# Optimization experiments

Hardware: AMD Instinct MI355X
Metric: run time of the kernel (lower is better)

The kernel has to match this reference:

```python
import jax, jax.numpy as jnp
import numpy as np

N = 8192
D = 128
NUM_CLASSES = 16
EPS = 1e-8  # torch cosine_similarity eps


def setup_inputs() -> dict:
    key = jax.random.key(0)
    k1, k2 = jax.random.split(key)
    inp = jax.random.normal(k1, (N, D), dtype=jnp.float32)
    targets = jax.random.randint(k2, (N,), 0, NUM_CLASSES, dtype=jnp.int64)
    temperature = jnp.asarray(0.5, dtype=jnp.float32)
    return {"input": inp, "targets": targets, "temperature": temperature}


def reference(input, targets, temperature):
    # clamp temperature to [0.1, 1.0] as the module does in forward
    temp = jnp.clip(temperature, 0.1, 1.0)

    # cosine similarity matrix [N, N]
    norms = jnp.maximum(jnp.linalg.norm(input, axis=1, keepdims=True), EPS)
    xn = input / norms
    sim = jnp.matmul(xn, xn.T) / temp          # [N, N]
    E = jnp.exp(sim)                            # [N, N]

    same = targets[:, None] == targets[None, :]  # [N, N] bool
    diag = jnp.diagonal(E)                       # exp(s_ii)
    pos = jnp.sum(jnp.where(same, E, 0.0), axis=1) - diag   # same-class, excl self
    tot = jnp.sum(E, axis=1) - diag                          # pos + neg
    per_sample_loss = -jnp.log(pos / tot)                    # [N]

    # per-class aggregation (segment sums with static num_segments)
    counts = jax.ops.segment_sum(jnp.ones_like(per_sample_loss), targets,
                                 num_segments=NUM_CLASSES)
    sums = jax.ops.segment_sum(per_sample_loss, targets,
                               num_segments=NUM_CLASSES)
    safe_counts = jnp.maximum(counts, 1.0)
    class_mean = sums / safe_counts

    # class weights: (1/count) normalized over present classes
    inv = jnp.where(counts > 0, 1.0 / safe_counts, 0.0)
    weights = inv / jnp.sum(inv)

    # only classes with more than one sample contribute
    valid = counts > 1
    weighted = jnp.where(valid, class_mean * weights, 0.0)
    n_valid = jnp.sum(valid.astype(jnp.float32))
    loss = jnp.sum(weighted) / n_valid
    return loss
```

## Files before the change

### kernel.cpp

```cpp
#include <hip/hip_runtime.h>

#define N 8192
#define D 128
#define NCLS 16
#define SLOT 512
#define RSTRIDE 256

typedef unsigned short u16;
typedef __attribute__((ext_vector_type(8))) short v8s;
typedef __attribute__((ext_vector_type(16))) float f32x16;

static __device__ inline u16 f2bf(float f) {
  unsigned int u = __builtin_bit_cast(unsigned int, f);
  unsigned int r = u + 0x7fffu + ((u >> 16) & 1u);
  return (u16)(r >> 16);
}

__global__ __launch_bounds__(256) void k_norm(float* __restrict__ buf) {
  int wave = threadIdx.x >> 6;
  int lane = threadIdx.x & 63;
  int row = blockIdx.x * 4 + wave;
  const float* p = buf + (size_t)row * D + lane * 2;
  float x = p[0], y = p[1];
  float ss = x * x + y * y;
#pragma unroll
  for (int m = 32; m >= 1; m >>= 1) ss += __shfl_xor(ss, m);
  float nrm = fmaxf(sqrtf(ss), 1e-8f);
  float inv = 1.0f / nrm;
  unsigned int u0 = (unsigned int)f2bf(x * inv);
  unsigned int u1 = (unsigned int)f2bf(y * inv);
  reinterpret_cast<unsigned int*>(buf)[(size_t)row * 128 + lane] = u0 | (u1 << 16);
}

__global__ __launch_bounds__(256, 2) void k_sim(float* __restrict__ buf,
                                                const int* __restrict__ tgt,
                                                const float* __restrict__ temp) {
  const int tid = threadIdx.x;
  const int wave = tid >> 6;
  const int lane = tid & 63;
  const int l31 = lane & 31;
  const int h = lane >> 5;

  const u16* xnb = reinterpret_cast<const u16*>(buf);

  const int bid = blockIdx.x;
  const int rowstrip = bid >> 2;
  const int cq = bid & 3;
  const int rwb = rowstrip * 64 + (wave >> 1) * 32;
  const int cbase = cq * 2048 + (wave & 1) * 32;

  float t = temp[0];
  t = fminf(fmaxf(t, 0.1f), 1.0f);
  const float scale = 1.4426950408889634f / t;

  v8s afrag[8];
  {
    const u16* ap = xnb + (size_t)(rwb + l31) * RSTRIDE + h * 8;
#pragma unroll
    for (int kk = 0; kk < 8; ++kk)
      afrag[kk] = *reinterpret_cast<const v8s*>(ap + kk * 16);
  }

  int trow[16];
#pragma unroll
  for (int r = 0; r < 16; ++r)
    trow[r] = tgt[rwb + ((r & 3) + 8 * (r >> 2) + 4 * h)];

  float tot_acc[16], pos_acc[16];
#pragma unroll
  for (int r = 0; r < 16; ++r) { tot_acc[r] = 0.f; pos_acc[r] = 0.f; }

  const u16* bp = xnb + (size_t)(cbase + l31) * RSTRIDE + h * 8;

  v8s bA[8], bB[8];
#pragma unroll
  for (int kk = 0; kk < 8; ++kk) bA[kk] = *reinterpret_cast<const v8s*>(bp + kk * 16);
#pragma unroll
  for (int kk = 0; kk < 8; ++kk) bB[kk] = *reinterpret_cast<const v8s*>(bp + 64 * RSTRIDE + kk * 16);

  auto tileCompute = [&](const v8s (&bf)[8], int c0) {
    f32x16 acc;
#pragma unroll
    for (int r = 0; r < 16; ++r) acc[r] = 0.f;
#pragma unroll
    for (int kk = 0; kk < 8; ++kk)
      acc = __builtin_amdgcn_mfma_f32_32x32x16_bf16(afrag[kk], bf[kk], acc, 0, 0, 0);
    int tcol = tgt[c0 + l31];
    if (c0 != rwb) {
#pragma unroll
      for (int r = 0; r < 16; ++r) {
        float e = exp2f(acc[r] * scale);
        tot_acc[r] += e;
        pos_acc[r] += (tcol == trow[r]) ? e : 0.f;
      }
    } else {
#pragma unroll
      for (int r = 0; r < 16; ++r) {
        float e = exp2f(acc[r] * scale);
        if (l31 == ((r & 3) + 8 * (r >> 2) + 4 * h)) e = 0.f;
        tot_acc[r] += e;
        pos_acc[r] += (tcol == trow[r]) ? e : 0.f;
      }
    }
  };

  for (int tt = 0; tt < 32; tt += 2) {
    tileCompute(bA, cbase + tt * 64);
    if (tt + 2 < 32) {
      const u16* q = bp + (size_t)(tt + 2) * 64 * RSTRIDE;
#pragma unroll
      for (int kk = 0; kk < 8; ++kk) bA[kk] = *reinterpret_cast<const v8s*>(q + kk * 16);
    }
    tileCompute(bB, cbase + (tt + 1) * 64);
    if (tt + 3 < 32) {
      const u16* q = bp + (size_t)(tt + 3) * 64 * RSTRIDE;
#pragma unroll
      for (int kk = 0; kk < 8; ++kk) bB[kk] = *reinterpret_cast<const v8s*>(q + kk * 16);
    }
  }

  __shared__ float red_pos[4][32];
  __shared__ float red_tot[4][32];
#pragma unroll
  for (int r = 0; r < 16; ++r) {
    float p = pos_acc[r], q = tot_acc[r];
#pragma unroll
    for (int m = 1; m <= 16; m <<= 1) {
      p += __shfl_xor(p, m);
      q += __shfl_xor(q, m);
    }
    if (l31 == 0) {
      int rl = (r & 3) + 8 * (r >> 2) + 4 * h;
      red_pos[wave][rl] = p;
      red_tot[wave][rl] = q;
    }
  }
  __syncthreads();
  if (tid < 64) {
    int g = tid >> 5, rl = tid & 31;
    int row = rowstrip * 64 + g * 32 + rl;
    float p = red_pos[2 * g][rl] + red_pos[2 * g + 1][rl];
    float q = red_tot[2 * g][rl] + red_tot[2 * g + 1][rl];
    float* slot = reinterpret_cast<float*>(reinterpret_cast<char*>(buf) + (size_t)row * SLOT + 256);
    slot[cq] = p;
    slot[4 + cq] = q;
  }
}

__global__ __launch_bounds__(128) void k_rowloss(float* __restrict__ buf,
                                                 const int* __restrict__ tgt) {
  __shared__ float cs[NCLS], cc[NCLS];
  int tid = threadIdx.x;
  int i = blockIdx.x * 128 + tid;
  if (tid < NCLS) { cs[tid] = 0.f; cc[tid] = 0.f; }
  __syncthreads();
  const float* slot = reinterpret_cast<const float*>(reinterpret_cast<const char*>(buf) + (size_t)i * SLOT + 256);
  float pos = slot[0] + slot[1] + slot[2] + slot[3];
  float tot = slot[4] + slot[5] + slot[6] + slot[7];
  float loss = logf(tot) - logf(pos);
  int c = tgt[i];
  atomicAdd(&cs[c], loss);
  atomicAdd(&cc[c], 1.0f);
  __syncthreads();
  if (tid < NCLS) {
    float* cls = reinterpret_cast<float*>(reinterpret_cast<char*>(buf) + (size_t)blockIdx.x * SLOT);
    cls[80 + tid] = cs[tid];
    cls[96 + tid] = cc[tid];
  }
}

__global__ __launch_bounds__(64) void k_final(const float* __restrict__ buf,
                                              float* __restrict__ out) {
  int c = threadIdx.x;
  float s = 0.f, n = 0.f;
  if (c < NCLS) {
#pragma unroll 4
    for (int b = 0; b < N / 128; ++b) {
      const float* cls = reinterpret_cast<const float*>(reinterpret_cast<const char*>(buf) + (size_t)b * SLOT);
      s += cls[80 + c];
      n += cls[96 + c];
    }
  }
  float safe = fmaxf(n, 1.0f);
  float mean = s / safe;
  float inv = (n > 0.5f) ? 1.0f / safe : 0.f;
  float valid = (n > 1.5f) ? 1.f : 0.f;
  float w = valid * mean * inv;
  float sinv = inv, sw = w, sv = valid;
#pragma unroll
  for (int m = 1; m <= 32; m <<= 1) {
    sinv += __shfl_xor(sinv, m);
    sw += __shfl_xor(sw, m);
    sv += __shfl_xor(sv, m);
  }
  if (c == 0) out[0] = sw / sinv / sv;
}

extern "C" void kernel_launch(void* const* d_in, const int* in_sizes, int n_in,
                              void* d_out, int out_size, void* d_ws, size_t ws_size,
                              hipStream_t stream) {
  float* buf = (float*)d_in[0];
  const int* tgt = (const int*)d_in[1];
  const float* temp = (const float*)d_in[2];
  float* out = (float*)d_out;
  (void)d_ws; (void)ws_size;

  k_norm<<<N / 4, 256, 0, stream>>>(buf);
  k_sim<<<512, 256, 0, stream>>>(buf, tgt, temp);
  k_rowloss<<<N / 128, 128, 0, stream>>>(buf, tgt);
  k_final<<<1, 64, 0, stream>>>(buf, out);
}
```

Baseline: 138.4 us.

## Fold temperature into normalization, retile sim kernel, fuse loss tail kernels

The normalization kernel now multiplies each row by sqrt(log2(e)/temp), so the sim kernel feeds the MFMA accumulators straight into exp2 with no per-element multiply. The sim kernel moves to 512-thread blocks covering 128 rows by 1024 columns, giving 8 column partials per row. The row-loss and final-reduction kernels merge into a single 1024-thread kernel, removing one launch and its round trip through global memory. The launch bound of (512, 4) caps registers hard, which can cause spills given the large fragment arrays. The folded scale is also rounded to bf16 along with the data, which slightly changes precision.

```diff
diff --git a/kernel.cpp b/kernel.cpp
--- a/kernel.cpp
+++ b/kernel.cpp
@@ -16,7 +16,8 @@
   return (u16)(r >> 16);
 }
 
-__global__ __launch_bounds__(256) void k_norm(float* __restrict__ buf) {
+__global__ __launch_bounds__(256) void k_norm(float* __restrict__ buf,
+                                              const float* __restrict__ temp) {
   int wave = threadIdx.x >> 6;
   int lane = threadIdx.x & 63;
   int row = blockIdx.x * 4 + wave;
@@ -25,16 +26,16 @@
   float ss = x * x + y * y;
 #pragma unroll
   for (int m = 32; m >= 1; m >>= 1) ss += __shfl_xor(ss, m);
-  float nrm = fmaxf(sqrtf(ss), 1e-8f);
-  float inv = 1.0f / nrm;
+  float t = fminf(fmaxf(temp[0], 0.1f), 1.0f);
+  float sc = sqrtf(1.4426950408889634f / t);
+  float inv = sc / fmaxf(sqrtf(ss), 1e-8f);
   unsigned int u0 = (unsigned int)f2bf(x * inv);
   unsigned int u1 = (unsigned int)f2bf(y * inv);
   reinterpret_cast<unsigned int*>(buf)[(size_t)row * 128 + lane] = u0 | (u1 << 16);
 }
 
-__global__ __launch_bounds__(256, 2) void k_sim(float* __restrict__ buf,
-                                                const int* __restrict__ tgt,
-                                                const float* __restrict__ temp) {
+__global__ __launch_bounds__(512, 4) void k_sim(float* __restrict__ buf,
+                                                const int* __restrict__ tgt) {
   const int tid = threadIdx.x;
   const int wave = tid >> 6;
   const int lane = tid & 63;
@@ -44,14 +45,10 @@
   const u16* xnb = reinterpret_cast<const u16*>(buf);
 
   const int bid = blockIdx.x;
-  const int rowstrip = bid >> 2;
-  const int cq = bid & 3;
-  const int rwb = rowstrip * 64 + (wave >> 1) * 32;
-  const int cbase = cq * 2048 + (wave & 1) * 32;
-
-  float t = temp[0];
-  t = fminf(fmaxf(t, 0.1f), 1.0f);
-  const float scale = 1.4426950408889634f / t;
+  const int rowstrip = bid >> 3;
+  const int cq = bid & 7;
+  const int rwb = rowstrip * 128 + (wave >> 1) * 32;
+  const int cbase = cq * 1024 + (wave & 1) * 32;
 
   v8s afrag[8];
   {
@@ -76,7 +73,7 @@
 #pragma unroll
   for (int kk = 0; kk < 8; ++kk) bA[kk] = *reinterpret_cast<const v8s*>(bp + kk * 16);
 #pragma unroll
-  for (int kk = 0; kk < 8; ++kk) bB[kk] = *reinterpret_cast<const v8s*>(bp + 64 * RSTRIDE + kk * 16);
+  for (int kk = 0; kk < 8; ++kk) bB[kk] = *reinterpret_cast<const v8s*>(bp + (size_t)64 * RSTRIDE + kk * 16);
 
   auto tileCompute = [&](const v8s (&bf)[8], int c0) {
     f32x16 acc;
@@ -89,14 +86,14 @@
     if (c0 != rwb) {
 #pragma unroll
       for (int r = 0; r < 16; ++r) {
-        float e = exp2f(acc[r] * scale);
+        float e = exp2f(acc[r]);
         tot_acc[r] += e;
         pos_acc[r] += (tcol == trow[r]) ? e : 0.f;
       }
     } else {
 #pragma unroll
       for (int r = 0; r < 16; ++r) {
-        float e = exp2f(acc[r] * scale);
+        float e = exp2f(acc[r]);
         if (l31 == ((r & 3) + 8 * (r >> 2) + 4 * h)) e = 0.f;
         tot_acc[r] += e;
         pos_acc[r] += (tcol == trow[r]) ? e : 0.f;
@@ -104,23 +101,23 @@
     }
   };
 
-  for (int tt = 0; tt < 32; tt += 2) {
+  for (int tt = 0; tt < 16; tt += 2) {
     tileCompute(bA, cbase + tt * 64);
-    if (tt + 2 < 32) {
+    if (tt + 2 < 16) {
       const u16* q = bp + (size_t)(tt + 2) * 64 * RSTRIDE;
 #pragma unroll
       for (int kk = 0; kk < 8; ++kk) bA[kk] = *reinterpret_cast<const v8s*>(q + kk * 16);
     }
     tileCompute(bB, cbase + (tt + 1) * 64);
-    if (tt + 3 < 32) {
+    if (tt + 3 < 16) {
       const u16* q = bp + (size_t)(tt + 3) * 64 * RSTRIDE;
 #pragma unroll
       for (int kk = 0; kk < 8; ++kk) bB[kk] = *reinterpret_cast<const v8s*>(q + kk * 16);
     }
   }
 
-  __shared__ float red_pos[4][32];
-  __shared__ float red_tot[4][32];
+  __shared__ float red_pos[8][32];
+  __shared__ float red_tot[8][32];
 #pragma unroll
   for (int r = 0; r < 16; ++r) {
     float p = pos_acc[r], q = tot_acc[r];
@@ -136,64 +133,56 @@
     }
   }
   __syncthreads();
-  if (tid < 64) {
+  if (tid < 128) {
     int g = tid >> 5, rl = tid & 31;
-    int row = rowstrip * 64 + g * 32 + rl;
+    int row = rowstrip * 128 + g * 32 + rl;
     float p = red_pos[2 * g][rl] + red_pos[2 * g + 1][rl];
     float q = red_tot[2 * g][rl] + red_tot[2 * g + 1][rl];
     float* slot = reinterpret_cast<float*>(reinterpret_cast<char*>(buf) + (size_t)row * SLOT + 256);
     slot[cq] = p;
-    slot[4 + cq] = q;
-  }
-}
-
-__global__ __launch_bounds__(128) void k_rowloss(float* __restrict__ buf,
-                                                 const int* __restrict__ tgt) {
+    slot[8 + cq] = q;
+  }
+}
+
+__global__ __launch_bounds__(1024) void k_tail(const float* __restrict__ buf,
+                                               const int* __restrict__ tgt,
+                                               float* __restrict__ out) {
   __shared__ float cs[NCLS], cc[NCLS];
   int tid = threadIdx.x;
-  int i = blockIdx.x * 128 + tid;
   if (tid < NCLS) { cs[tid] = 0.f; cc[tid] = 0.f; }
   __syncthreads();
-  const float* slot = reinterpret_cast<const float*>(reinterpret_cast<const char*>(buf) + (size_t)i * SLOT + 256);
-  float pos = slot[0] + slot[1] + slot[2] + slot[3];
-  float tot = slot[4] + slot[5] + slot[6] + slot[7];
-  float loss = logf(tot) - logf(pos);
-  int c = tgt[i];
-  atomicAdd(&cs[c], loss);
-  atomicAdd(&cc[c], 1.0f);
+#pragma unroll
+  for (int j = 0; j < 8; ++j) {
+    int row = j * 1024 + tid;
+    const float4* s4 = reinterpret_cast<const float4*>(
+        reinterpret_cast<const char*>(buf) + (size_t)row * SLOT + 256);
+    float4 a = s4[0], b = s4[1], c4 = s4[2], d4 = s4[3];
+    float pos = a.x + a.y + a.z + a.w + b.x + b.y + b.z + b.w;
+    float tot = c4.x + c4.y + c4.z + c4.w + d4.x + d4.y + d4.z + d4.w;
+    float loss = logf(tot) - logf(pos);
+    int c = tgt[row];
+    atomicAdd(&cs[c], loss);
+    atomicAdd(&cc[c], 1.0f);
+  }
   __syncthreads();
-  if (tid < NCLS) {
-    float* cls = reinterpret_cast<float*>(reinterpret_cast<char*>(buf) + (size_t)blockIdx.x * SLOT);
-    cls[80 + tid] = cs[tid];
-    cls[96 + tid] = cc[tid];
-  }
-}
-
-__global__ __launch_bounds__(64) void k_final(const float* __restrict__ buf,
-                                              float* __restrict__ out) {
-  int c = threadIdx.x;
-  float s = 0.f, n = 0.f;
-  if (c < NCLS) {
-#pragma unroll 4
-    for (int b = 0; b < N / 128; ++b) {
-      const float* cls = reinterpret_cast<const float*>(reinterpret_cast<const char*>(buf) + (size_t)b * SLOT);
-      s += cls[80 + c];
-      n += cls[96 + c];
-    }
-  }
-  float safe = fmaxf(n, 1.0f);
-  float mean = s / safe;
-  float inv = (n > 0.5f) ? 1.0f / safe : 0.f;
-  float valid = (n > 1.5f) ? 1.f : 0.f;
-  float w = valid * mean * inv;
-  float sinv = inv, sw = w, sv = valid;
-#pragma unroll
-  for (int m = 1; m <= 32; m <<= 1) {
-    sinv += __shfl_xor(sinv, m);
-    sw += __shfl_xor(sw, m);
-    sv += __shfl_xor(sv, m);
-  }
-  if (c == 0) out[0] = sw / sinv / sv;
+  if (tid < 64) {
+    int c = tid;
+    float s = 0.f, n = 0.f;
+    if (c < NCLS) { s = cs[c]; n = cc[c]; }
+    float safe = fmaxf(n, 1.0f);
+    float mean = s / safe;
+    float inv = (n > 0.5f) ? 1.0f / safe : 0.f;
+    float valid = (n > 1.5f) ? 1.f : 0.f;
+    float w = (n > 1.5f) ? mean * inv : 0.f;
+    float sinv = inv, sw = w, sv = valid;
+#pragma unroll
+    for (int m = 1; m <= 32; m <<= 1) {
+      sinv += __shfl_xor(sinv, m);
+      sw += __shfl_xor(sw, m);
+      sv += __shfl_xor(sv, m);
+    }
+    if (c == 0) out[0] = sw / sinv / sv;
+  }
 }
 
 extern "C" void kernel_launch(void* const* d_in, const int* in_sizes, int n_in,
@@ -205,8 +194,7 @@
   float* out = (float*)d_out;
   (void)d_ws; (void)ws_size;
 
-  k_norm<<<N / 4, 256, 0, stream>>>(buf);
-  k_sim<<<512, 256, 0, stream>>>(buf, tgt, temp);
-  k_rowloss<<<N / 128, 128, 0, stream>>>(buf, tgt);
-  k_final<<<1, 64, 0, stream>>>(buf, out);
-}
+  k_norm<<<N / 4, 256, 0, stream>>>(buf, temp);
+  k_sim<<<512, 512, 0, stream>>>(buf, tgt);
+  k_tail<<<1, 1024, 0, stream>>>(buf, tgt, out);
+}
```

New measurement: 338.5 us. 145% more time.
